# Optimization experiments

Hardware: AMD Instinct MI355X
Metric: run time of the kernel (lower is better)

The kernel has to match this reference:

```python
import jax, jax.numpy as jnp
import numpy as np

D = 2048
N_PASSES = 2
TOKENS = 16384


def _wht_matrix(d):
    # Sylvester construction of the (unnormalized) Walsh-Hadamard matrix.
    h = np.array([[1.0]], dtype=np.float32)
    while h.shape[0] < d:
        h = np.block([[h, h], [h, -h]])
    return jnp.asarray(h)


def setup_inputs() -> dict:
    key = jax.random.key(0)
    kx, ks = jax.random.split(key)
    x = jax.random.normal(kx, (TOKENS, D), dtype=jnp.float32)
    # random +/-1 sign arrays, one per pass (buffers in the torch module)
    signs = (2 * jax.random.randint(ks, (N_PASSES, D), 0, 2) - 1).astype(jnp.int32)
    wht_mat = _wht_matrix(D)
    return {"x": x, "signs": signs, "wht_mat": wht_mat}


def reference(x, signs, wht_mat):
    # Cascaded SRHT: (sign flip -> dense WHT matmul) x n_passes, scale fused at end.
    final_scale = jnp.asarray(1.0 / (D ** (N_PASSES / 2.0)), dtype=x.dtype)
    s = signs.astype(x.dtype)
    out = x
    for i in range(N_PASSES):
        out = out * s[i]          # [tokens, d] broadcast sign flip
        out = out @ wht_mat       # [tokens, d] x [d, d]
    return out * final_scale
```

## Files before the change

kernel.cpp:

```cpp
#include <hip/hip_runtime.h>

#define DIM 2048

typedef unsigned int uint2v __attribute__((ext_vector_type(2)));

__device__ __forceinline__ float4 sign_flip(float4 v, uint4 s) {
  float4 r;
  r.x = __uint_as_float(__float_as_uint(v.x) ^ (s.x & 0x80000000u));
  r.y = __uint_as_float(__float_as_uint(v.y) ^ (s.y & 0x80000000u));
  r.z = __uint_as_float(__float_as_uint(v.z) ^ (s.z & 0x80000000u));
  r.w = __uint_as_float(__float_as_uint(v.w) ^ (s.w & 0x80000000u));
  return r;
}

#define BFLY(a, b) { float _t = (a); (a) = _t + (b); (b) = _t - (b); }

__device__ __forceinline__ void bf4_pair(float4 &a, float4 &b) {
  BFLY(a.x, b.x); BFLY(a.y, b.y); BFLY(a.z, b.z); BFLY(a.w, b.w);
}

__device__ __forceinline__ void bf_comps(float4 &a) {
  BFLY(a.x, a.y); BFLY(a.z, a.w);
  BFLY(a.x, a.z); BFLY(a.y, a.w);
}

__device__ __forceinline__ void bf_oct(float4 v[8]) {
  bf4_pair(v[0], v[1]); bf4_pair(v[2], v[3]);
  bf4_pair(v[4], v[5]); bf4_pair(v[6], v[7]);
  bf4_pair(v[0], v[2]); bf4_pair(v[1], v[3]);
  bf4_pair(v[4], v[6]); bf4_pair(v[5], v[7]);
  bf4_pair(v[0], v[4]); bf4_pair(v[1], v[5]);
  bf4_pair(v[2], v[6]); bf4_pair(v[3], v[7]);
}

template <int CTRL>
__device__ __forceinline__ float dpp_mov(float x) {
  return __int_as_float(
      __builtin_amdgcn_mov_dpp(__float_as_int(x), CTRL, 0xF, 0xF, true));
}

template <int CTRL>
__device__ __forceinline__ void dpp_stage(float4 v[8], float sgn) {
  #pragma unroll
  for (int i = 0; i < 8; ++i) {
    float px = dpp_mov<CTRL>(v[i].x);
    float py = dpp_mov<CTRL>(v[i].y);
    float pz = dpp_mov<CTRL>(v[i].z);
    float pw = dpp_mov<CTRL>(v[i].w);
    v[i].x = fmaf(sgn, v[i].x, px);
    v[i].y = fmaf(sgn, v[i].y, py);
    v[i].z = fmaf(sgn, v[i].z, pz);
    v[i].w = fmaf(sgn, v[i].w, pw);
  }
}

template <int PAT>
__device__ __forceinline__ float swz_mov(float x) {
  return __int_as_float(__builtin_amdgcn_ds_swizzle(__float_as_int(x), PAT));
}

template <int PAT>
__device__ __forceinline__ void swz_stage(float4 v[8], float sgn) {
  #pragma unroll
  for (int i = 0; i < 8; ++i) {
    float px = swz_mov<PAT>(v[i].x);
    float py = swz_mov<PAT>(v[i].y);
    float pz = swz_mov<PAT>(v[i].z);
    float pw = swz_mov<PAT>(v[i].w);
    v[i].x = fmaf(sgn, v[i].x, px);
    v[i].y = fmaf(sgn, v[i].y, py);
    v[i].z = fmaf(sgn, v[i].z, pz);
    v[i].w = fmaf(sgn, v[i].w, pw);
  }
}

__device__ __forceinline__ float pl32_bfly(float x, float sgn) {
  uint2v r = __builtin_amdgcn_permlane32_swap(
      __float_as_uint(x), __float_as_uint(x), false, false);
  return fmaf(sgn, __uint_as_float(r[1]), __uint_as_float(r[0]));
}

__device__ __forceinline__ void pl32_stage(float4 v[8], float sgn) {
  #pragma unroll
  for (int i = 0; i < 8; ++i) {
    v[i].x = pl32_bfly(v[i].x, sgn);
    v[i].y = pl32_bfly(v[i].y, sgn);
    v[i].z = pl32_bfly(v[i].z, sgn);
    v[i].w = pl32_bfly(v[i].w, sgn);
  }
}

__global__ __launch_bounds__(256, 8) void srht2_kernel(
    const float* __restrict__ x, const int* __restrict__ signs,
    float* __restrict__ out, int nrows) {
  const int lane = threadIdx.x & 63;
  const int wv   = threadIdx.x >> 6;
  const int row  = blockIdx.x * 4 + wv;
  if (row >= nrows) return;

  const float sgn1  = (lane & 1)  ? -1.0f : 1.0f;
  const float sgn2  = (lane & 2)  ? -1.0f : 1.0f;
  const float sgn4  = (lane & 4)  ? -1.0f : 1.0f;
  const float sgn8  = (lane & 8)  ? -1.0f : 1.0f;
  const float sgn16 = (lane & 16) ? -1.0f : 1.0f;
  const float sgn32 = (lane & 32) ? -1.0f : 1.0f;

  const float4* __restrict__ xr = (const float4*)(x + (size_t)row * DIM);
  const uint4*  __restrict__ s0 = (const uint4*)signs;
  const uint4*  __restrict__ s1 = (const uint4*)(signs + DIM);

  float4 v[8];
  #pragma unroll
  for (int c = 0; c < 8; ++c) {
    v[c] = xr[c * 64 + lane];
    v[c] = sign_flip(v[c], s0[c * 64 + lane]);
  }

  #pragma unroll
  for (int c = 0; c < 8; ++c) bf_comps(v[c]);
  dpp_stage<0xB1>(v, sgn1);
  dpp_stage<0x4E>(v, sgn2);
  swz_stage<0x101F>(v, sgn4);
  swz_stage<0x201F>(v, sgn8);
  swz_stage<0x401F>(v, sgn16);
  pl32_stage(v, sgn32);
  bf_oct(v);

  #pragma unroll
  for (int c = 0; c < 8; ++c) v[c] = sign_flip(v[c], s1[c * 64 + lane]);

  #pragma unroll
  for (int c = 0; c < 8; ++c) bf_comps(v[c]);
  dpp_stage<0xB1>(v, sgn1);
  dpp_stage<0x4E>(v, sgn2);
  swz_stage<0x101F>(v, sgn4);
  swz_stage<0x201F>(v, sgn8);
  swz_stage<0x401F>(v, sgn16);
  pl32_stage(v, sgn32);
  bf_oct(v);

  const float sc = 1.0f / 2048.0f;
  float4* __restrict__ orow = (float4*)(out + (size_t)row * DIM);
  #pragma unroll
  for (int c = 0; c < 8; ++c) {
    float4 t = v[c];
    t.x *= sc; t.y *= sc; t.z *= sc; t.w *= sc;
    orow[c * 64 + lane] = t;
  }
}

extern "C" void kernel_launch(void* const* d_in, const int* in_sizes, int n_in,
                              void* d_out, int out_size, void* d_ws, size_t ws_size,
                              hipStream_t stream) {
  const float* x     = (const float*)d_in[0];
  const int*   signs = (const int*)d_in[1];
  float*       out   = (float*)d_out;
  const int nrows   = in_sizes[0] / DIM;
  const int nblocks = nrows / 4;
  hipLaunchKernelGGL(srht2_kernel, dim3(nblocks), dim3(256), 0, stream,
                     x, signs, out, nrows);
}
```

Before: 265.7 us.

## Replace ds_swizzle butterfly stages with LDS transpose exchange and permlane16

Drops the three ds_swizzle butterfly stages (lane bits 2,3,4) per pass. Lane bit 4 is now handled by permlane16_swap, and lane bits 2-3 by an LDS exchange that moves those bits into the register index, so the following butterflies run in registers. The second pass reads signs at permuted indices to match the new layout. This adds LDS traffic, waitcnt fences and shared memory per block, and the launch_bounds occupancy hint is removed.

```diff
diff --git a/kernel.cpp b/kernel.cpp
--- a/kernel.cpp
+++ b/kernel.cpp
@@ -33,6 +33,13 @@
   bf4_pair(v[2], v[6]); bf4_pair(v[3], v[7]);
 }
 
+__device__ __forceinline__ void bf_oct12(float4 v[8]) {
+  bf4_pair(v[0], v[1]); bf4_pair(v[2], v[3]);
+  bf4_pair(v[4], v[5]); bf4_pair(v[6], v[7]);
+  bf4_pair(v[0], v[2]); bf4_pair(v[1], v[3]);
+  bf4_pair(v[4], v[6]); bf4_pair(v[5], v[7]);
+}
+
 template <int CTRL>
 __device__ __forceinline__ float dpp_mov(float x) {
   return __int_as_float(
@@ -54,23 +61,19 @@
   }
 }
 
-template <int PAT>
-__device__ __forceinline__ float swz_mov(float x) {
-  return __int_as_float(__builtin_amdgcn_ds_swizzle(__float_as_int(x), PAT));
+__device__ __forceinline__ float pl16_bfly(float x, float sgn) {
+  uint2v r = __builtin_amdgcn_permlane16_swap(
+      __float_as_uint(x), __float_as_uint(x), false, false);
+  return fmaf(sgn, __uint_as_float(r[1]), __uint_as_float(r[0]));
 }
 
-template <int PAT>
-__device__ __forceinline__ void swz_stage(float4 v[8], float sgn) {
+__device__ __forceinline__ void pl16_stage(float4 v[8], float sgn) {
   #pragma unroll
   for (int i = 0; i < 8; ++i) {
-    float px = swz_mov<PAT>(v[i].x);
-    float py = swz_mov<PAT>(v[i].y);
-    float pz = swz_mov<PAT>(v[i].z);
-    float pw = swz_mov<PAT>(v[i].w);
-    v[i].x = fmaf(sgn, v[i].x, px);
-    v[i].y = fmaf(sgn, v[i].y, py);
-    v[i].z = fmaf(sgn, v[i].z, pz);
-    v[i].w = fmaf(sgn, v[i].w, pw);
+    v[i].x = pl16_bfly(v[i].x, sgn);
+    v[i].y = pl16_bfly(v[i].y, sgn);
+    v[i].z = pl16_bfly(v[i].z, sgn);
+    v[i].w = pl16_bfly(v[i].w, sgn);
   }
 }
 
@@ -90,18 +93,41 @@
   }
 }
 
-__global__ __launch_bounds__(256, 8) void srht2_kernel(
+__device__ __forceinline__ void lds_fence() {
+  asm volatile("s_waitcnt lgkmcnt(0)" ::: "memory");
+}
+
+__device__ __forceinline__ void xchg(float4* __restrict__ W, float4 v[8],
+                                     int lane) {
+  const int m  = (lane >> 2) & 3;
+  const int ls = lane & ~12;
+  #pragma unroll
+  for (int half = 0; half < 2; ++half) {
+    const int cs = half * 4;
+    #pragma unroll
+    for (int c2 = 0; c2 < 4; ++c2)
+      W[c2 * 64 + (lane ^ ((c2 & 1) << 2))] = v[cs + c2];
+    lds_fence();
+    #pragma unroll
+    for (int c2 = 0; c2 < 4; ++c2)
+      v[cs + c2] = W[m * 64 + ((ls | (c2 << 2)) ^ ((m & 1) << 2))];
+    lds_fence();
+  }
+}
+
+__global__ __launch_bounds__(256) void srht2_kernel(
     const float* __restrict__ x, const int* __restrict__ signs,
     float* __restrict__ out, int nrows) {
+  __shared__ __align__(16) float4 lds[4][256];
   const int lane = threadIdx.x & 63;
   const int wv   = threadIdx.x >> 6;
   const int row  = blockIdx.x * 4 + wv;
   if (row >= nrows) return;
 
+  float4* __restrict__ W = lds[wv];
+
   const float sgn1  = (lane & 1)  ? -1.0f : 1.0f;
   const float sgn2  = (lane & 2)  ? -1.0f : 1.0f;
-  const float sgn4  = (lane & 4)  ? -1.0f : 1.0f;
-  const float sgn8  = (lane & 8)  ? -1.0f : 1.0f;
   const float sgn16 = (lane & 16) ? -1.0f : 1.0f;
   const float sgn32 = (lane & 32) ? -1.0f : 1.0f;
 
@@ -111,33 +137,35 @@
 
   float4 v[8];
   #pragma unroll
-  for (int c = 0; c < 8; ++c) {
-    v[c] = xr[c * 64 + lane];
-    v[c] = sign_flip(v[c], s0[c * 64 + lane]);
-  }
+  for (int c = 0; c < 8; ++c) v[c] = xr[c * 64 + lane];
 
+  #pragma unroll
+  for (int c = 0; c < 8; ++c) v[c] = sign_flip(v[c], s0[c * 64 + lane]);
   #pragma unroll
   for (int c = 0; c < 8; ++c) bf_comps(v[c]);
   dpp_stage<0xB1>(v, sgn1);
   dpp_stage<0x4E>(v, sgn2);
-  swz_stage<0x101F>(v, sgn4);
-  swz_stage<0x201F>(v, sgn8);
-  swz_stage<0x401F>(v, sgn16);
+  pl16_stage(v, sgn16);
   pl32_stage(v, sgn32);
   bf_oct(v);
 
+  xchg(W, v, lane);
+  bf_oct12(v);
+
+  const int sb = (lane & 3) | ((lane >> 4) << 4) | (((lane >> 2) & 3) << 6);
   #pragma unroll
-  for (int c = 0; c < 8; ++c) v[c] = sign_flip(v[c], s1[c * 64 + lane]);
-
+  for (int c = 0; c < 8; ++c)
+    v[c] = sign_flip(v[c], s1[sb + ((c & 3) << 2) + ((c >> 2) << 8)]);
   #pragma unroll
   for (int c = 0; c < 8; ++c) bf_comps(v[c]);
   dpp_stage<0xB1>(v, sgn1);
   dpp_stage<0x4E>(v, sgn2);
-  swz_stage<0x101F>(v, sgn4);
-  swz_stage<0x201F>(v, sgn8);
-  swz_stage<0x401F>(v, sgn16);
+  pl16_stage(v, sgn16);
   pl32_stage(v, sgn32);
   bf_oct(v);
+
+  xchg(W, v, lane);
+  bf_oct12(v);
 
   const float sc = 1.0f / 2048.0f;
   float4* __restrict__ orow = (float4*)(out + (size_t)row * DIM);
```

After: 241.8 us. 9.0% less time.
